# Kernel optimization log

Measured on AMD Instinct MI355X. Metric: run time of the kernel, lower is better.

## Reference

```python
import math
import jax, jax.numpy as jnp
import numpy as np

NUM_HEADS = 32
KV_HEADS = 8
HEAD_DIM = 128
BLOCK_SIZE = 16
MAX_CTX = 2048
BSZ = 64
BLOCKS_PER_SEQ = MAX_CTX // BLOCK_SIZE  # 128
NUM_BLOCKS = BSZ * BLOCKS_PER_SEQ       # 8192


def setup_inputs() -> dict:
    key = jax.random.key(0)
    k1, k2, k3, k4 = jax.random.split(key, 4)
    query = jax.random.normal(k1, (BSZ, NUM_HEADS, HEAD_DIM), dtype=jnp.float32)
    key_cache = jax.random.normal(k2, (NUM_BLOCKS, KV_HEADS, BLOCK_SIZE, HEAD_DIM), dtype=jnp.float32)
    value_cache = jax.random.normal(k3, (NUM_BLOCKS, KV_HEADS, BLOCK_SIZE, HEAD_DIM), dtype=jnp.float32)
    # each sequence owns a contiguous run of blocks (valid paged layout)
    block_tables = jnp.arange(NUM_BLOCKS, dtype=jnp.int32).reshape(BSZ, BLOCKS_PER_SEQ)
    # per-sequence context lengths in [1, MAX_CTX]
    input_lens = jax.random.randint(k4, (BSZ,), 1, MAX_CTX + 1, dtype=jnp.int32)
    return {
        "query": query,
        "key_cache": key_cache,
        "value_cache": value_cache,
        "block_tables": block_tables,
        "input_lens": input_lens,
    }


def reference(query, key_cache, value_cache, block_tables, input_lens):
    """Paged single-query cached-KV attention with GQA (decode path of _IPEXAttention).

    query:       [bsz, num_heads, head_dim]  (one new token per sequence)
    key_cache:   [num_blocks, kv_heads, block_size, head_dim]
    value_cache: [num_blocks, kv_heads, block_size, head_dim]
    block_tables:[bsz, blocks_per_seq] int32
    input_lens:  [bsz] int32 valid context length per sequence
    returns:     [bsz, num_heads * head_dim]
    """
    bsz, nh, hd = query.shape
    groups = nh // KV_HEADS  # kv_head_mapping = arange(KV_HEADS).repeat_interleave(groups)
    scale = 1.0 / math.sqrt(hd)

    # Gather paged KV: [bsz, blocks, kvh, bs, hd] -> [bsz, kvh, S, hd]
    k = key_cache[block_tables].transpose(0, 2, 1, 3, 4).reshape(bsz, KV_HEADS, -1, hd)
    v = value_cache[block_tables].transpose(0, 2, 1, 3, 4).reshape(bsz, KV_HEADS, -1, hd)
    S = k.shape[2]

    # GQA: query heads grouped by their kv head
    q = query.reshape(bsz, KV_HEADS, groups, hd)

    scores = jnp.einsum("bkgd,bksd->bkgs", q, k) * scale  # [bsz, kvh, groups, S]
    valid = jnp.arange(S, dtype=jnp.int32)[None, :] < input_lens[:, None]  # [bsz, S]
    neg = jnp.finfo(scores.dtype).min
    scores = jnp.where(valid[:, None, None, :], scores, neg)
    probs = jax.nn.softmax(scores, axis=-1)

    out = jnp.einsum("bkgs,bksd->bkgd", probs, v)  # [bsz, kvh, groups, hd]
    # attn_output.reshape(-1, num_heads * head_dim) as in the torch module
    return out.reshape(bsz, nh * hd)
```

## Files before the change

### kernel.cpp

```cpp
#include <hip/hip_runtime.h>
#include <math.h>

#define NUM_HEADS 32
#define KV_HEADS 8
#define GROUPS 4
#define HEAD_DIM 128
#define BLOCK_SIZE 16
#define MAX_CTX 2048
#define BSZ 64
#define BLOCKS_PER_SEQ 128

#define CHUNK_BLOCKS 16
#define CHUNK_TOKENS (CHUNK_BLOCKS * BLOCK_SIZE)
#define NCHUNK (MAX_CTX / CHUNK_TOKENS)
#define REC_STRIDE 520

__global__ __launch_bounds__(256, 3)
void attn_partial_kernel(const float* __restrict__ q,
                         const float* __restrict__ kcache,
                         const float* __restrict__ vcache,
                         const int*   __restrict__ btab,
                         const int*   __restrict__ lens,
                         float*       __restrict__ part)
{
    const int chunk = blockIdx.x;
    const int kvh   = blockIdx.y;
    const int seq   = blockIdx.z;

    const int len = lens[seq];
    if (chunk * CHUNK_TOKENS >= len) return;

    const int tid  = threadIdx.x;
    const int wave = tid >> 6;
    const int lane = tid & 63;
    const int g    = lane >> 4;
    const int u    = lane & 15;

    const float qs = 0.08838834764831845f * 1.44269504088896340736f;

    float4 qa[GROUPS], qb[GROUPS];
    const float* qbase = q + ((size_t)seq * NUM_HEADS + (size_t)kvh * GROUPS) * HEAD_DIM;
#pragma unroll
    for (int h = 0; h < GROUPS; ++h) {
        float4 t = *(const float4*)(qbase + h * HEAD_DIM + 4 * u);
        qa[h] = make_float4(t.x * qs, t.y * qs, t.z * qs, t.w * qs);
        t = *(const float4*)(qbase + h * HEAD_DIM + 64 + 4 * u);
        qb[h] = make_float4(t.x * qs, t.y * qs, t.z * qs, t.w * qs);
    }

    float  m[GROUPS], l[GROUPS];
    float4 oa[GROUPS], ob[GROUPS];
#pragma unroll
    for (int h = 0; h < GROUPS; ++h) {
        m[h] = -INFINITY; l[h] = 0.f;
        oa[h] = make_float4(0.f, 0.f, 0.f, 0.f);
        ob[h] = make_float4(0.f, 0.f, 0.f, 0.f);
    }

    const int nblk   = (len + BLOCK_SIZE - 1) / BLOCK_SIZE;
    const int bstart = chunk * CHUNK_BLOCKS;
    const int bend   = min(bstart + CHUNK_BLOCKS, nblk);

    for (int b = bstart + wave; b < bend; b += 4) {
        const int phys = btab[seq * BLOCKS_PER_SEQ + b];
        const size_t slice = ((size_t)phys * KV_HEADS + kvh) * (BLOCK_SIZE * HEAD_DIM);
        const float* kblk = kcache + slice;
        const float* vblk = vcache + slice;

        float  s[4][GROUPS];
        float4 va[4], vb[4];
#pragma unroll
        for (int j = 0; j < 4; ++j) {
            const int off = (4 * j + g) * HEAD_DIM + 4 * u;
            float4 ka = *(const float4*)(kblk + off);
            float4 kb = *(const float4*)(kblk + off + 64);
            va[j] = *(const float4*)(vblk + off);
            vb[j] = *(const float4*)(vblk + off + 64);
#pragma unroll
            for (int h = 0; h < GROUPS; ++h) {
                s[j][h] = ka.x * qa[h].x + ka.y * qa[h].y + ka.z * qa[h].z + ka.w * qa[h].w
                        + kb.x * qb[h].x + kb.y * qb[h].y + kb.z * qb[h].z + kb.w * qb[h].w;
            }
        }

#pragma unroll
        for (int d = 1; d < 16; d <<= 1) {
#pragma unroll
            for (int j = 0; j < 4; ++j)
#pragma unroll
                for (int h = 0; h < GROUPS; ++h)
                    s[j][h] += __shfl_xor(s[j][h], d, 64);
        }

        const int tb = b * BLOCK_SIZE + g;
#pragma unroll
        for (int j = 0; j < 4; ++j) {
            if (tb + 4 * j >= len) {
#pragma unroll
                for (int h = 0; h < GROUPS; ++h) s[j][h] = -INFINITY;
            }
        }

#pragma unroll
        for (int h = 0; h < GROUPS; ++h) {
            float bm = fmaxf(fmaxf(s[0][h], s[1][h]), fmaxf(s[2][h], s[3][h]));
            bm = fmaxf(bm, __shfl_xor(bm, 16, 64));
            bm = fmaxf(bm, __shfl_xor(bm, 32, 64));
            const float mn    = fmaxf(m[h], bm);
            const float alpha = exp2f(m[h] - mn);
            l[h] *= alpha;
            oa[h].x *= alpha; oa[h].y *= alpha; oa[h].z *= alpha; oa[h].w *= alpha;
            ob[h].x *= alpha; ob[h].y *= alpha; ob[h].z *= alpha; ob[h].w *= alpha;
            m[h] = mn;
        }

#pragma unroll
        for (int j = 0; j < 4; ++j) {
#pragma unroll
            for (int h = 0; h < GROUPS; ++h) {
                const float p = exp2f(s[j][h] - m[h]);
                l[h] += p;
                oa[h].x += p * va[j].x; oa[h].y += p * va[j].y;
                oa[h].z += p * va[j].z; oa[h].w += p * va[j].w;
                ob[h].x += p * vb[j].x; ob[h].y += p * vb[j].y;
                ob[h].z += p * vb[j].z; ob[h].w += p * vb[j].w;
            }
        }
    }

#pragma unroll
    for (int d = 16; d <= 32; d <<= 1) {
#pragma unroll
        for (int h = 0; h < GROUPS; ++h) {
            const float mo = __shfl_xor(m[h], d, 64);
            const float mn = fmaxf(m[h], mo);
            const float w  = (m[h] == -INFINITY) ? 0.f : exp2f(m[h] - mn);
            float ls = l[h] * w;
            l[h] = ls + __shfl_xor(ls, d, 64);
            oa[h].x *= w; oa[h].y *= w; oa[h].z *= w; oa[h].w *= w;
            ob[h].x *= w; ob[h].y *= w; ob[h].z *= w; ob[h].w *= w;
            oa[h].x += __shfl_xor(oa[h].x, d, 64);
            oa[h].y += __shfl_xor(oa[h].y, d, 64);
            oa[h].z += __shfl_xor(oa[h].z, d, 64);
            oa[h].w += __shfl_xor(oa[h].w, d, 64);
            ob[h].x += __shfl_xor(ob[h].x, d, 64);
            ob[h].y += __shfl_xor(ob[h].y, d, 64);
            ob[h].z += __shfl_xor(ob[h].z, d, 64);
            ob[h].w += __shfl_xor(ob[h].w, d, 64);
            m[h] = mn;
        }
    }

    __shared__ float o_lds[4][GROUPS][HEAD_DIM];
    __shared__ float m_lds[4][GROUPS];
    __shared__ float l_lds[4][GROUPS];
    if (g == 0) {
#pragma unroll
        for (int h = 0; h < GROUPS; ++h) {
            *(float4*)&o_lds[wave][h][4 * u]      = oa[h];
            *(float4*)&o_lds[wave][h][64 + 4 * u] = ob[h];
        }
        if (u == 0) {
#pragma unroll
            for (int h = 0; h < GROUPS; ++h) { m_lds[wave][h] = m[h]; l_lds[wave][h] = l[h]; }
        }
    }
    __syncthreads();

    float* rec = part + (((size_t)(seq * KV_HEADS + kvh)) * NCHUNK + chunk) * REC_STRIDE;
#pragma unroll
    for (int r = 0; r < 2; ++r) {
        const int e = tid + r * 256;
        const int h = e >> 7;
        const int d = e & 127;
        float mstar = fmaxf(fmaxf(m_lds[0][h], m_lds[1][h]),
                            fmaxf(m_lds[2][h], m_lds[3][h]));
        float num = 0.f, L = 0.f;
#pragma unroll
        for (int w = 0; w < 4; ++w) {
            float mw = m_lds[w][h];
            float ww = (mw == -INFINITY) ? 0.f : exp2f(mw - mstar);
            num += o_lds[w][h][d] * ww;
            L   += l_lds[w][h] * ww;
        }
        rec[e] = num;
        if (d == 0) { rec[512 + h] = mstar; rec[516 + h] = L; }
    }
}

__global__ __launch_bounds__(256)
void attn_reduce_kernel(const float* __restrict__ part,
                        const int*   __restrict__ lens,
                        float*       __restrict__ out)
{
    const int kvh = blockIdx.x & (KV_HEADS - 1);
    const int seq = blockIdx.x / KV_HEADS;
    const int len = lens[seq];
    const int nlive = (len + CHUNK_TOKENS - 1) / CHUNK_TOKENS;

    const float* base = part + ((size_t)(seq * KV_HEADS + kvh)) * NCHUNK * REC_STRIDE;
    const int tid = threadIdx.x;

#pragma unroll
    for (int r = 0; r < 2; ++r) {
        const int e = tid + r * 256;
        const int h = e >> 7;
        const int d = e & 127;

        float mstar = -INFINITY;
        for (int ch = 0; ch < nlive; ++ch)
            mstar = fmaxf(mstar, base[ch * REC_STRIDE + 512 + h]);

        float num = 0.f, L = 0.f;
        for (int ch = 0; ch < nlive; ++ch) {
            const float* r0 = base + ch * REC_STRIDE;
            float ww = exp2f(r0[512 + h] - mstar);
            num += r0[e] * ww;
            L   += r0[516 + h] * ww;
        }
        out[(size_t)seq * (NUM_HEADS * HEAD_DIM) + (kvh * GROUPS + h) * HEAD_DIM + d] = num / L;
    }
}

extern "C" void kernel_launch(void* const* d_in, const int* in_sizes, int n_in,
                              void* d_out, int out_size, void* d_ws, size_t ws_size,
                              hipStream_t stream) {
    const float* q    = (const float*)d_in[0];
    const float* kc   = (const float*)d_in[1];
    const float* vc   = (const float*)d_in[2];
    const int*   bt   = (const int*)d_in[3];
    const int*   lens = (const int*)d_in[4];
    float* out  = (float*)d_out;
    float* part = (float*)d_ws;

    dim3 g1(NCHUNK, KV_HEADS, BSZ);
    attn_partial_kernel<<<g1, 256, 0, stream>>>(q, kc, vc, bt, lens, part);

    dim3 g2(BSZ * KV_HEADS);
    attn_reduce_kernel<<<g2, 256, 0, stream>>>(part, lens, out);
}
```

Measured before the change: 939.6 us.

## Use DPP row reductions, per-lane-group softmax, and preloaded block table entries

Measured after the change: 920.7 us. 1.02x faster.

```diff
diff --git a/kernel.cpp b/kernel.cpp
--- a/kernel.cpp
+++ b/kernel.cpp
@@ -14,6 +14,19 @@
 #define CHUNK_TOKENS (CHUNK_BLOCKS * BLOCK_SIZE)
 #define NCHUNK (MAX_CTX / CHUNK_TOKENS)
 #define REC_STRIDE 520
+
+template <int CTRL>
+__device__ __forceinline__ float dpp_add(float x) {
+    int y = __builtin_amdgcn_update_dpp(0, __float_as_int(x), CTRL, 0xF, 0xF, true);
+    return x + __int_as_float(y);
+}
+__device__ __forceinline__ float row_allsum(float x) {
+    x = dpp_add<0x128>(x);
+    x = dpp_add<0x124>(x);
+    x = dpp_add<0x122>(x);
+    x = dpp_add<0x121>(x);
+    return x;
+}
 
 __global__ __launch_bounds__(256, 3)
 void attn_partial_kernel(const float* __restrict__ q,
@@ -61,9 +74,16 @@
     const int bstart = chunk * CHUNK_BLOCKS;
     const int bend   = min(bstart + CHUNK_BLOCKS, nblk);
 
-    for (int b = bstart + wave; b < bend; b += 4) {
-        const int phys = btab[seq * BLOCKS_PER_SEQ + b];
-        const size_t slice = ((size_t)phys * KV_HEADS + kvh) * (BLOCK_SIZE * HEAD_DIM);
+    int physv[4];
+#pragma unroll
+    for (int k = 0; k < 4; ++k)
+        physv[k] = btab[seq * BLOCKS_PER_SEQ + bstart + wave + 4 * k];
+
+#pragma unroll 1
+    for (int k = 0; k < 4; ++k) {
+        const int b = bstart + wave + 4 * k;
+        if (b >= bend) break;
+        const size_t slice = ((size_t)physv[k] * KV_HEADS + kvh) * (BLOCK_SIZE * HEAD_DIM);
         const float* kblk = kcache + slice;
         const float* vblk = vcache + slice;
 
@@ -84,13 +104,10 @@
         }
 
 #pragma unroll
-        for (int d = 1; d < 16; d <<= 1) {
-#pragma unroll
-            for (int j = 0; j < 4; ++j)
-#pragma unroll
-                for (int h = 0; h < GROUPS; ++h)
-                    s[j][h] += __shfl_xor(s[j][h], d, 64);
-        }
+        for (int j = 0; j < 4; ++j)
+#pragma unroll
+            for (int h = 0; h < GROUPS; ++h)
+                s[j][h] = row_allsum(s[j][h]);
 
         const int tb = b * BLOCK_SIZE + g;
 #pragma unroll
@@ -103,27 +120,24 @@
 
 #pragma unroll
         for (int h = 0; h < GROUPS; ++h) {
-            float bm = fmaxf(fmaxf(s[0][h], s[1][h]), fmaxf(s[2][h], s[3][h]));
-            bm = fmaxf(bm, __shfl_xor(bm, 16, 64));
-            bm = fmaxf(bm, __shfl_xor(bm, 32, 64));
-            const float mn    = fmaxf(m[h], bm);
-            const float alpha = exp2f(m[h] - mn);
-            l[h] *= alpha;
-            oa[h].x *= alpha; oa[h].y *= alpha; oa[h].z *= alpha; oa[h].w *= alpha;
-            ob[h].x *= alpha; ob[h].y *= alpha; ob[h].z *= alpha; ob[h].w *= alpha;
-            m[h] = mn;
-        }
-
-#pragma unroll
-        for (int j = 0; j < 4; ++j) {
-#pragma unroll
-            for (int h = 0; h < GROUPS; ++h) {
-                const float p = exp2f(s[j][h] - m[h]);
-                l[h] += p;
-                oa[h].x += p * va[j].x; oa[h].y += p * va[j].y;
-                oa[h].z += p * va[j].z; oa[h].w += p * va[j].w;
-                ob[h].x += p * vb[j].x; ob[h].y += p * vb[j].y;
-                ob[h].z += p * vb[j].z; ob[h].w += p * vb[j].w;
+            const float bm = fmaxf(fmaxf(s[0][h], s[1][h]), fmaxf(s[2][h], s[3][h]));
+            const float mn = fmaxf(m[h], bm);
+            if (mn > -INFINITY) {
+                const float alpha = exp2f(m[h] - mn);
+                m[h] = mn;
+                float lh = l[h] * alpha;
+                oa[h].x *= alpha; oa[h].y *= alpha; oa[h].z *= alpha; oa[h].w *= alpha;
+                ob[h].x *= alpha; ob[h].y *= alpha; ob[h].z *= alpha; ob[h].w *= alpha;
+#pragma unroll
+                for (int j = 0; j < 4; ++j) {
+                    const float p = exp2f(s[j][h] - mn);
+                    lh += p;
+                    oa[h].x += p * va[j].x; oa[h].y += p * va[j].y;
+                    oa[h].z += p * va[j].z; oa[h].w += p * va[j].w;
+                    ob[h].x += p * vb[j].x; ob[h].y += p * vb[j].y;
+                    ob[h].z += p * vb[j].z; ob[h].w += p * vb[j].w;
+                }
+                l[h] = lh;
             }
         }
     }
```
